# Optimization experiments

Measured on AMD Instinct MI355X. Metric: run time of the kernel, lower is better.

Reference implementation:

```python
import jax, jax.numpy as jnp
import numpy as np

N_NODES = 100000
N_EDGES = 1600000
N_REL = 8
N_HEADS = 4
IN_FEAT = 128
OUT_FEAT = 64
D_HEAD = OUT_FEAT // N_HEADS
LEAKY_SLOPE = 0.2


def setup_inputs() -> dict:
    key = jax.random.key(0)
    ks = jax.random.split(key, 8)
    inputs = jax.random.normal(ks[0], (N_NODES, IN_FEAT), dtype=jnp.float32)
    conv_weights = jax.random.normal(ks[1], (N_REL, N_HEADS, IN_FEAT, D_HEAD), dtype=jnp.float32) * (1.0 / np.sqrt(IN_FEAT))
    attn_l = jax.random.normal(ks[2], (N_REL, N_HEADS, D_HEAD), dtype=jnp.float32) * (1.0 / np.sqrt(D_HEAD))
    attn_r = jax.random.normal(ks[3], (N_REL, N_HEADS, D_HEAD), dtype=jnp.float32) * (1.0 / np.sqrt(D_HEAD))
    h_bias = jax.random.normal(ks[4], (OUT_FEAT,), dtype=jnp.float32)
    src_idx = jax.random.randint(ks[5], (N_EDGES,), 0, N_NODES, dtype=jnp.int64) if jax.config.jax_enable_x64 else jax.random.randint(ks[5], (N_EDGES,), 0, N_NODES, dtype=jnp.int32)
    dst_idx = jax.random.randint(ks[6], (N_EDGES,), 0, N_NODES, dtype=src_idx.dtype)
    rel_idx = jax.random.randint(ks[7], (N_EDGES,), 0, N_REL, dtype=src_idx.dtype)
    return {"inputs": inputs, "conv_weights": conv_weights, "attn_l": attn_l,
            "attn_r": attn_r, "h_bias": h_bias, "src_idx": src_idx,
            "dst_idx": dst_idx, "rel_idx": rel_idx}


def reference(inputs, conv_weights, attn_l, attn_r, h_bias, src_idx, dst_idx, rel_idx):
    N = inputs.shape[0]
    # Per-node per-relation projection: [N, R, H, Dh]
    # (equivalent math to the per-relation grouped matmul over unique nodes)
    proj = jnp.einsum('ni,rhid->nrhd', inputs, conv_weights)
    # Gather per-edge src/dst projected features under the edge's relation: [E, H, Dh]
    feat_src = proj[src_idx, rel_idx]
    feat_dst = proj[dst_idx, rel_idx]
    # Attention logits per edge/head: [E, H]
    el = jnp.sum(feat_src * attn_l[rel_idx], axis=-1)
    er = jnp.sum(feat_dst * attn_r[rel_idx], axis=-1)
    score = jax.nn.leaky_relu(el + er, negative_slope=LEAKY_SLOPE)
    # Edge softmax over incoming edges of each destination node (per head)
    smax = jax.ops.segment_max(score, dst_idx, num_segments=N)        # [N, H]
    e = jnp.exp(score - smax[dst_idx])                                # [E, H]
    denom = jax.ops.segment_sum(e, dst_idx, num_segments=N)          # [N, H]
    alpha = e / denom[dst_idx]                                        # [E, H]
    # Weighted aggregation of src features to dst nodes: [N, H, Dh]
    h = jax.ops.segment_sum(alpha[..., None] * feat_src, dst_idx, num_segments=N)
    h = h.reshape(N, OUT_FEAT) + h_bias
    return h
```

## Files before the change

kernel.cpp:

```cpp
#include <hip/hip_runtime.h>
#include <hip/hip_bf16.h>


#define NN 100000
#define NNP 100096
#define NE 1600000
#define NH 4
#define INF_ 128
#define DH 16
#define NCOL 576
#define LEAKY 0.2f
#define NBUCK 391
#define BSHIFT 8
#define CHUNK 4096
#define CAP 5120
#define GEMM_BLOCKS 782
#define WEXT_BLOCKS 288

typedef __hip_bfloat16 bf16;
typedef __attribute__((ext_vector_type(8))) short bf16x8;
typedef __attribute__((ext_vector_type(4))) short bf16x4;
typedef __attribute__((ext_vector_type(4))) float f32x4;

static __device__ __forceinline__ short f2bs(float x) {
    bf16 b = __float2bfloat16(x);
    return *reinterpret_cast<short*>(&b);
}
static __device__ __forceinline__ float bflo(unsigned u) { return __uint_as_float(u << 16); }
static __device__ __forceinline__ float bfhi(unsigned u) { return __uint_as_float(u & 0xffff0000u); }

__global__ void build_wextT(const float* __restrict__ W, const float* __restrict__ al,
                            const float* __restrict__ ar, short* __restrict__ wxt2,
                            int* __restrict__ gCursor) {
    if (blockIdx.x >= WEXT_BLOCKS) {
        int i = (blockIdx.x - WEXT_BLOCKS) * 256 + threadIdx.x;
        if (i < NBUCK) gCursor[i] = 0;
        return;
    }
    int idx = blockIdx.x * 256 + threadIdx.x;
    int e = idx & 7, lane = (idx >> 3) & 63, ct = (idx >> 9) & 3, ks = (idx >> 11) & 3, cb = idx >> 13;
    int g = lane >> 4, r = lane & 15;
    int c = cb * 64 + ct * 16 + r;
    int k = ks * 32 + g * 8 + e;
    float v;
    if (c < 512) {
        int rr = c >> 6, rem = c & 63, h = rem >> 4, d = rem & 15;
        v = W[((rr * NH + h) * INF_ + k) * DH + d];
    } else {
        int rh = c - 512;
        const float* a = al;
        if (rh >= 32) { rh -= 32; a = ar; }
        int rr = rh >> 2, h = rh & 3;
        const float* wp = &W[((rr * NH + h) * INF_ + k) * DH];
        const float* ap = &a[(rr * NH + h) * DH];
        float s = 0.f;
        #pragma unroll
        for (int d = 0; d < DH; ++d) s += wp[d] * ap[d];
        v = s;
    }
    wxt2[idx] = f2bs(v);
}

__global__ __launch_bounds__(256) void gemm_fused(
    const float* __restrict__ A, const short* __restrict__ WxT2,
    bf16* __restrict__ projR, float* __restrict__ elr,
    const int* __restrict__ src, const int* __restrict__ dst, const int* __restrict__ rel,
    int* __restrict__ gCursor, int* __restrict__ pairbuf) {
    __shared__ short As[16384];
    int t = threadIdx.x;

    if (blockIdx.x >= GEMM_BLOCKS) {
        int* hist = (int*)As;
        int blk = blockIdx.x - GEMM_BLOCKS;
        for (int i = t; i < NBUCK; i += 256) hist[i] = 0;
        __syncthreads();
        int base = blk * CHUNK;
        #pragma unroll
        for (int j = 0; j < CHUNK / 256; ++j) {
            int e = base + j * 256 + t;
            if (e < NE) atomicAdd(&hist[dst[e] >> BSHIFT], 1);
        }
        __syncthreads();
        for (int i = t; i < NBUCK; i += 256) {
            int v = hist[i];
            hist[i] = v ? (i * CAP + atomicAdd(&gCursor[i], v)) : 0;
        }
        __syncthreads();
        #pragma unroll
        for (int j = 0; j < CHUNK / 256; ++j) {
            int e = base + j * 256 + t;
            if (e < NE) {
                int d = dst[e];
                int b = d >> BSHIFT;
                int rec = ((d & 255) << 20) | (src[e] * 8 + rel[e]);
                int pos = atomicAdd(&hist[b], 1);
                pairbuf[pos] = rec;
            }
        }
        return;
    }

    int wv = t >> 6, lane = t & 63;
    int n0 = blockIdx.x * 128;
    int g = lane >> 4, r = lane & 15;

    #pragma unroll
    for (int j = 0; j < 8; ++j) {
        int i = j * 256 + t;
        int row = i >> 4, c8 = i & 15;
        int gr = n0 + row;
        bf16x8 v;
        if (gr < NN) {
            float4 f0 = *(const float4*)&A[gr * INF_ + c8 * 8];
            float4 f1 = *(const float4*)&A[gr * INF_ + c8 * 8 + 4];
            v[0] = f2bs(f0.x); v[1] = f2bs(f0.y); v[2] = f2bs(f0.z); v[3] = f2bs(f0.w);
            v[4] = f2bs(f1.x); v[5] = f2bs(f1.y); v[6] = f2bs(f1.z); v[7] = f2bs(f1.w);
        } else {
            v = (bf16x8)(short)0;
        }
        *(bf16x8*)&As[(row * 16 + (c8 ^ (row & 7))) * 8] = v;
    }
    __syncthreads();

    bf16x8 afr[2][4];
    #pragma unroll
    for (int nt = 0; nt < 2; ++nt) {
        int row = wv * 32 + nt * 16 + r;
        #pragma unroll
        for (int ks = 0; ks < 4; ++ks)
            afr[nt][ks] = *(const bf16x8*)&As[(row * 16 + ((ks * 4 + g) ^ (r & 7))) * 8];
    }
    __syncthreads();
    short* Csh = &As[wv * 4096];
    float* Csf = (float*)Csh;
    int n0w = n0 + wv * 32;

    for (int cb = 0; cb < 9; ++cb) {
        f32x4 acc[2][4] = {};
        #pragma unroll
        for (int ks = 0; ks < 4; ++ks) {
            #pragma unroll
            for (int ct = 0; ct < 4; ++ct) {
                bf16x8 b = *(const bf16x8*)&WxT2[(((cb * 4 + ks) * 4 + ct) * 64 + lane) * 8];
                acc[0][ct] = __builtin_amdgcn_mfma_f32_16x16x32_bf16(b, afr[0][ks], acc[0][ct], 0, 0, 0);
                acc[1][ct] = __builtin_amdgcn_mfma_f32_16x16x32_bf16(b, afr[1][ks], acc[1][ct], 0, 0, 0);
            }
        }
        if (cb < 8) {
            #pragma unroll
            for (int nt = 0; nt < 2; ++nt) {
                int rr = nt * 16 + r;
                #pragma unroll
                for (int ct = 0; ct < 4; ++ct) {
                    bf16x4 p;
                    p[0] = f2bs(acc[nt][ct][0]); p[1] = f2bs(acc[nt][ct][1]);
                    p[2] = f2bs(acc[nt][ct][2]); p[3] = f2bs(acc[nt][ct][3]);
                    *(bf16x4*)&Csh[rr * 64 + (((ct * 4 + g) ^ ((rr & 7) << 1)) << 2)] = p;
                }
            }
            __builtin_amdgcn_wave_barrier();
            size_t base = ((size_t)cb * NN + n0w) * 64;
            #pragma unroll
            for (int q = 0; q < 4; ++q) {
                int rr = (lane >> 3) + q * 8;
                if (n0w + rr < NN) {
                    bf16x8 vv = *(const bf16x8*)&Csh[rr * 64 + (((lane & 7) ^ (rr & 7)) << 3)];
                    *(bf16x8*)&((short*)projR)[base + q * 512 + lane * 8] = vv;
                }
            }
            __builtin_amdgcn_wave_barrier();
        } else {
            #pragma unroll
            for (int nt = 0; nt < 2; ++nt) {
                int rr = nt * 16 + r;
                #pragma unroll
                for (int ct = 0; ct < 4; ++ct)
                    *(f32x4*)&Csf[rr * 64 + (((ct * 4 + g) ^ ((rr & 7) << 1)) << 2)] = acc[nt][ct];
            }
            __builtin_amdgcn_wave_barrier();
            #pragma unroll
            for (int q = 0; q < 8; ++q) {
                int rr = (lane >> 4) + q * 4;
                if (n0w + rr < NN) {
                    f32x4 vv = *(const f32x4*)&Csf[rr * 64 + (((lane & 15) ^ ((rr & 7) << 1)) << 2)];
                    *(f32x4*)&elr[(size_t)n0w * 64 + q * 256 + lane * 4] = vv;
                }
            }
        }
    }
}

__global__ __launch_bounds__(256) void exact_place(
    const int* __restrict__ gCursor, const int* __restrict__ pairbuf,
    int2* __restrict__ offdeg, int2* __restrict__ rec2) {
    __shared__ int hist[256];
    __shared__ int tsum[256];
    int b = blockIdx.x, t = threadIdx.x;
    int start = b * CAP, cnt = gCursor[b];
    hist[t] = 0;
    __syncthreads();
    for (int i = t; i < cnt; i += 256) atomicAdd(&hist[pairbuf[start + i] >> 20], 1);
    __syncthreads();
    int own = hist[t];
    tsum[t] = own;
    __syncthreads();
    for (int st = 1; st < 256; st <<= 1) {
        int y = (t >= st) ? tsum[t - st] : 0;
        __syncthreads();
        tsum[t] += y;
        __syncthreads();
    }
    int excl = start + tsum[t] - own;
    int node = b * 256 + t;
    if (node < NN) offdeg[node] = make_int2(excl, own);
    __syncthreads();
    hist[t] = excl;
    __syncthreads();
    for (int i = t; i < cnt; i += 256) {
        int rec = pairbuf[start + i];
        int pos = atomicAdd(&hist[rec >> 20], 1);
        int sr = rec & 0xFFFFF;
        rec2[pos] = make_int2((sr >> 3) * 64 + (sr & 7) * 4,
                              (sr & 7) * (NN * 64) + (sr >> 3) * 64);
    }
}

__global__ __launch_bounds__(256) void agg(
    const int2* __restrict__ offdeg, const int2* __restrict__ rec2,
    const float* __restrict__ elr, const bf16* __restrict__ projR,
    const float* __restrict__ bias, float* __restrict__ out) {
    __shared__ float s_alpha[4][64][4];
    __shared__ int   s_pidx[4][64];
    __shared__ float s_er[4][32];
    int wv = threadIdx.x >> 6, lane = threadIdx.x & 63;
    int d = blockIdx.x * 4 + wv;
    if (d >= NN) return;
    int2 od = offdeg[d];
    int off = od.x, deg = od.y;
    int end = off + deg;

    if (lane < 32) s_er[wv][lane] = elr[d * 64 + 32 + lane];
    __builtin_amdgcn_wave_barrier();
    asm volatile("s_waitcnt lgkmcnt(0)" ::: "memory");

    if (deg == 0) {
        if (lane < 32) {
            float2 bb = *(const float2*)&bias[lane * 2];
            *(float2*)&out[d * 64 + lane * 2] = bb;
        }
    } else if (deg <= 64) {
        int i = off + lane;
        float e0 = 0.f, e1 = 0.f, e2 = 0.f, e3 = 0.f;
        int pidx = 0;
        if (i < end) {
            int2 rv = rec2[i];
            pidx = rv.y;
            float4 el4 = *(const float4*)&elr[rv.x];
            int erb = rv.x & 63;
            float x;
            x = el4.x + s_er[wv][erb + 0]; x = x > 0.f ? x : LEAKY * x; e0 = __expf(x);
            x = el4.y + s_er[wv][erb + 1]; x = x > 0.f ? x : LEAKY * x; e1 = __expf(x);
            x = el4.z + s_er[wv][erb + 2]; x = x > 0.f ? x : LEAKY * x; e2 = __expf(x);
            x = el4.w + s_er[wv][erb + 3]; x = x > 0.f ? x : LEAKY * x; e3 = __expf(x);
        }
        s_pidx[wv][lane] = pidx;
        *(float4*)&s_alpha[wv][lane][0] = make_float4(e0, e1, e2, e3);
        __builtin_amdgcn_wave_barrier();
        asm volatile("s_waitcnt lgkmcnt(0)" ::: "memory");

        int col2 = (lane & 31) * 2;
        int hl = lane >> 5;
        int h2 = (lane & 31) >> 3;
        float acc0 = 0.f, acc1 = 0.f, dsum = 0.f;
        int j = 0;
        for (; j + 8 <= deg; j += 8) {
            unsigned uu[4];
            #pragma unroll
            for (int p = 0; p < 4; ++p) {
                int myp = s_pidx[wv][j + 2 * p + hl];
                uu[p] = *(const unsigned*)&projR[myp + col2];
            }
            #pragma unroll
            for (int p = 0; p < 4; ++p) {
                float a_self = s_alpha[wv][j + 2 * p + hl][h2];
                float a_oth  = s_alpha[wv][j + 2 * p + 1 - hl][h2];
                unsigned uo = __shfl_xor((int)uu[p], 32);
                acc0 = fmaf(a_self, bflo(uu[p]), acc0);
                acc1 = fmaf(a_self, bfhi(uu[p]), acc1);
                acc0 = fmaf(a_oth, bflo(uo), acc0);
                acc1 = fmaf(a_oth, bfhi(uo), acc1);
                dsum += a_self + a_oth;
            }
        }
        for (; j + 2 <= deg; j += 2) {
            int myp = s_pidx[wv][j + hl];
            unsigned u = *(const unsigned*)&projR[myp + col2];
            float a_self = s_alpha[wv][j + hl][h2];
            float a_oth  = s_alpha[wv][j + 1 - hl][h2];
            unsigned uo = __shfl_xor((int)u, 32);
            acc0 = fmaf(a_self, bflo(u), acc0);
            acc1 = fmaf(a_self, bfhi(u), acc1);
            acc0 = fmaf(a_oth, bflo(uo), acc0);
            acc1 = fmaf(a_oth, bfhi(uo), acc1);
            dsum += a_self + a_oth;
        }
        if (j < deg) {
            int myp = s_pidx[wv][j];
            unsigned u = *(const unsigned*)&projR[myp + col2];
            float a = s_alpha[wv][j][h2];
            acc0 = fmaf(a, bflo(u), acc0);
            acc1 = fmaf(a, bfhi(u), acc1);
            dsum += a;
        }
        if (lane < 32) {
            float inv = 1.0f / dsum;
            float2 bb = *(const float2*)&bias[col2];
            float2 o;
            o.x = acc0 * inv + bb.x;
            o.y = acc1 * inv + bb.y;
            *(float2*)&out[d * 64 + col2] = o;
        }
    } else {
        int c = lane, h = c >> 4;
        float dsum0 = 0.f, dsum1 = 0.f, dsum2 = 0.f, dsum3 = 0.f;
        for (int i = off + lane; i < end; i += 64) {
            int2 rv = rec2[i];
            float4 el4 = *(const float4*)&elr[rv.x];
            int erb = rv.x & 63;
            float x;
            x = el4.x + s_er[wv][erb + 0]; x = x > 0.f ? x : LEAKY * x; dsum0 += __expf(x);
            x = el4.y + s_er[wv][erb + 1]; x = x > 0.f ? x : LEAKY * x; dsum1 += __expf(x);
            x = el4.z + s_er[wv][erb + 2]; x = x > 0.f ? x : LEAKY * x; dsum2 += __expf(x);
            x = el4.w + s_er[wv][erb + 3]; x = x > 0.f ? x : LEAKY * x; dsum3 += __expf(x);
        }
        #pragma unroll
        for (int m = 32; m; m >>= 1) {
            dsum0 += __shfl_xor(dsum0, m, 64);
            dsum1 += __shfl_xor(dsum1, m, 64);
            dsum2 += __shfl_xor(dsum2, m, 64);
            dsum3 += __shfl_xor(dsum3, m, 64);
        }
        float dh = (h == 0) ? dsum0 : (h == 1) ? dsum1 : (h == 2) ? dsum2 : dsum3;
        float rd = 1.0f / dh;
        float acc = 0.f;
        for (int i = off; i < end; ++i) {
            int2 rv = rec2[i];
            float x = elr[rv.x + h] + s_er[wv][(rv.x & 63) + h];
            x = x > 0.f ? x : LEAKY * x;
            acc = fmaf(__expf(x) * rd, __bfloat162float(projR[rv.y + c]), acc);
        }
        out[d * 64 + c] = acc + bias[c];
    }
}

extern "C" void kernel_launch(void* const* d_in, const int* in_sizes, int n_in,
                              void* d_out, int out_size, void* d_ws, size_t ws_size,
                              hipStream_t stream) {
    const float* inputs = (const float*)d_in[0];
    const float* convw  = (const float*)d_in[1];
    const float* attn_l = (const float*)d_in[2];
    const float* attn_r = (const float*)d_in[3];
    const float* h_bias = (const float*)d_in[4];
    const int*   src    = (const int*)d_in[5];
    const int*   dst    = (const int*)d_in[6];
    const int*   rel    = (const int*)d_in[7];
    float* out = (float*)d_out;

    char* ws = (char*)d_ws;
    size_t o = 0;
    bf16* projR = (bf16*)(ws + o);  o += 102400000ull;
    float* elr  = (float*)(ws + o); o += 25600000ull;
    short* wxt2 = (short*)(ws + o); o += 147456;
    int2* offdeg = (int2*)(ws + o); o += 800768;
    int* gCursor = (int*)(ws + o);  o += 2048;
    int* pairbuf = (int*)(ws + o);  o += (size_t)NBUCK * CAP * 4;
    int2* rec2   = (int2*)(ws + o); o += (size_t)NBUCK * CAP * 8;

    hipLaunchKernelGGL(build_wextT, dim3(WEXT_BLOCKS + 2), dim3(256), 0, stream,
                       convw, attn_l, attn_r, wxt2, gCursor);
    hipLaunchKernelGGL(gemm_fused, dim3(GEMM_BLOCKS + NBUCK), dim3(256), 0, stream,
                       inputs, wxt2, projR, elr, src, dst, rel, gCursor, pairbuf);
    hipLaunchKernelGGL(exact_place, dim3(NBUCK), dim3(256), 0, stream, gCursor, pairbuf, offdeg, rec2);
    hipLaunchKernelGGL(agg, dim3(25000), dim3(256), 0, stream, offdeg, rec2, elr, projR, h_bias, out);
}
```

Measured before the change: 142.5 us.

## Store attention logits in bf16 and shrink edge records to one int

The per-node attention logit table (el/er) is now written by the GEMM in bf16 instead of fp32, which halves its footprint and unifies the epilogue path with the projection stores. The per-edge record drops from int2 to a single int, and the aggregation kernel recomputes the projection gather offset from it arithmetically. This cuts write traffic in the GEMM and in edge placement, and read traffic in the aggregation gathers. The cost is lower precision in the softmax logits and a few extra integer ops per edge.

```diff
diff --git a/kernel.cpp b/kernel.cpp
--- a/kernel.cpp
+++ b/kernel.cpp
@@ -28,6 +28,9 @@
 }
 static __device__ __forceinline__ float bflo(unsigned u) { return __uint_as_float(u << 16); }
 static __device__ __forceinline__ float bfhi(unsigned u) { return __uint_as_float(u & 0xffff0000u); }
+static __device__ __forceinline__ float b2f(short us) {
+    return __uint_as_float(((unsigned)(unsigned short)us) << 16);
+}
 
 __global__ void build_wextT(const float* __restrict__ W, const float* __restrict__ al,
                             const float* __restrict__ ar, short* __restrict__ wxt2,
@@ -63,7 +66,7 @@
 
 __global__ __launch_bounds__(256) void gemm_fused(
     const float* __restrict__ A, const short* __restrict__ WxT2,
-    bf16* __restrict__ projR, float* __restrict__ elr,
+    short* __restrict__ projR, short* __restrict__ elrb,
     const int* __restrict__ src, const int* __restrict__ dst, const int* __restrict__ rel,
     int* __restrict__ gCursor, int* __restrict__ pairbuf) {
     __shared__ short As[16384];
@@ -132,7 +135,6 @@
     }
     __syncthreads();
     short* Csh = &As[wv * 4096];
-    float* Csf = (float*)Csh;
     int n0w = n0 + wv * 32;
 
     for (int cb = 0; cb < 9; ++cb) {
@@ -146,53 +148,35 @@
                 acc[1][ct] = __builtin_amdgcn_mfma_f32_16x16x32_bf16(b, afr[1][ks], acc[1][ct], 0, 0, 0);
             }
         }
-        if (cb < 8) {
+        #pragma unroll
+        for (int nt = 0; nt < 2; ++nt) {
+            int rr = nt * 16 + r;
             #pragma unroll
-            for (int nt = 0; nt < 2; ++nt) {
-                int rr = nt * 16 + r;
-                #pragma unroll
-                for (int ct = 0; ct < 4; ++ct) {
-                    bf16x4 p;
-                    p[0] = f2bs(acc[nt][ct][0]); p[1] = f2bs(acc[nt][ct][1]);
-                    p[2] = f2bs(acc[nt][ct][2]); p[3] = f2bs(acc[nt][ct][3]);
-                    *(bf16x4*)&Csh[rr * 64 + (((ct * 4 + g) ^ ((rr & 7) << 1)) << 2)] = p;
-                }
-            }
-            __builtin_amdgcn_wave_barrier();
-            size_t base = ((size_t)cb * NN + n0w) * 64;
-            #pragma unroll
-            for (int q = 0; q < 4; ++q) {
-                int rr = (lane >> 3) + q * 8;
-                if (n0w + rr < NN) {
-                    bf16x8 vv = *(const bf16x8*)&Csh[rr * 64 + (((lane & 7) ^ (rr & 7)) << 3)];
-                    *(bf16x8*)&((short*)projR)[base + q * 512 + lane * 8] = vv;
-                }
-            }
-            __builtin_amdgcn_wave_barrier();
-        } else {
-            #pragma unroll
-            for (int nt = 0; nt < 2; ++nt) {
-                int rr = nt * 16 + r;
-                #pragma unroll
-                for (int ct = 0; ct < 4; ++ct)
-                    *(f32x4*)&Csf[rr * 64 + (((ct * 4 + g) ^ ((rr & 7) << 1)) << 2)] = acc[nt][ct];
-            }
-            __builtin_amdgcn_wave_barrier();
-            #pragma unroll
-            for (int q = 0; q < 8; ++q) {
-                int rr = (lane >> 4) + q * 4;
-                if (n0w + rr < NN) {
-                    f32x4 vv = *(const f32x4*)&Csf[rr * 64 + (((lane & 15) ^ ((rr & 7) << 1)) << 2)];
-                    *(f32x4*)&elr[(size_t)n0w * 64 + q * 256 + lane * 4] = vv;
-                }
-            }
-        }
+            for (int ct = 0; ct < 4; ++ct) {
+                bf16x4 p;
+                p[0] = f2bs(acc[nt][ct][0]); p[1] = f2bs(acc[nt][ct][1]);
+                p[2] = f2bs(acc[nt][ct][2]); p[3] = f2bs(acc[nt][ct][3]);
+                *(bf16x4*)&Csh[rr * 64 + (((ct * 4 + g) ^ ((rr & 7) << 1)) << 2)] = p;
+            }
+        }
+        __builtin_amdgcn_wave_barrier();
+        short* dstbase = (cb < 8) ? &projR[((size_t)cb * NN + n0w) * 64]
+                                  : &elrb[(size_t)n0w * 64];
+        #pragma unroll
+        for (int q = 0; q < 4; ++q) {
+            int rr = (lane >> 3) + q * 8;
+            if (n0w + rr < NN) {
+                bf16x8 vv = *(const bf16x8*)&Csh[rr * 64 + (((lane & 7) ^ (rr & 7)) << 3)];
+                *(bf16x8*)&dstbase[q * 512 + lane * 8] = vv;
+            }
+        }
+        __builtin_amdgcn_wave_barrier();
     }
 }
 
 __global__ __launch_bounds__(256) void exact_place(
     const int* __restrict__ gCursor, const int* __restrict__ pairbuf,
-    int2* __restrict__ offdeg, int2* __restrict__ rec2) {
+    int2* __restrict__ offdeg, int* __restrict__ rec) {
     __shared__ int hist[256];
     __shared__ int tsum[256];
     int b = blockIdx.x, t = threadIdx.x;
@@ -217,17 +201,16 @@
     hist[t] = excl;
     __syncthreads();
     for (int i = t; i < cnt; i += 256) {
-        int rec = pairbuf[start + i];
-        int pos = atomicAdd(&hist[rec >> 20], 1);
-        int sr = rec & 0xFFFFF;
-        rec2[pos] = make_int2((sr >> 3) * 64 + (sr & 7) * 4,
-                              (sr & 7) * (NN * 64) + (sr >> 3) * 64);
+        int rc = pairbuf[start + i];
+        int pos = atomicAdd(&hist[rc >> 20], 1);
+        int sr = rc & 0xFFFFF;
+        rec[pos] = (sr >> 3) * 64 + (sr & 7) * 4;
     }
 }
 
 __global__ __launch_bounds__(256) void agg(
-    const int2* __restrict__ offdeg, const int2* __restrict__ rec2,
-    const float* __restrict__ elr, const bf16* __restrict__ projR,
+    const int2* __restrict__ offdeg, const int* __restrict__ rec,
+    const short* __restrict__ elrb, const bf16* __restrict__ projR,
     const float* __restrict__ bias, float* __restrict__ out) {
     __shared__ float s_alpha[4][64][4];
     __shared__ int   s_pidx[4][64];
@@ -239,7 +222,7 @@
     int off = od.x, deg = od.y;
     int end = off + deg;
 
-    if (lane < 32) s_er[wv][lane] = elr[d * 64 + 32 + lane];
+    if (lane < 32) s_er[wv][lane] = b2f(elrb[d * 64 + 32 + lane]);
     __builtin_amdgcn_wave_barrier();
     asm volatile("s_waitcnt lgkmcnt(0)" ::: "memory");
 
@@ -253,15 +236,15 @@
         float e0 = 0.f, e1 = 0.f, e2 = 0.f, e3 = 0.f;
         int pidx = 0;
         if (i < end) {
-            int2 rv = rec2[i];
-            pidx = rv.y;
-            float4 el4 = *(const float4*)&elr[rv.x];
-            int erb = rv.x & 63;
+            int rv = rec[i];
+            pidx = ((rv & 63) >> 2) * (NN * 64) + (rv >> 6) * 64;
+            bf16x4 el4 = *(const bf16x4*)&elrb[rv];
+            int erb = rv & 63;
             float x;
-            x = el4.x + s_er[wv][erb + 0]; x = x > 0.f ? x : LEAKY * x; e0 = __expf(x);
-            x = el4.y + s_er[wv][erb + 1]; x = x > 0.f ? x : LEAKY * x; e1 = __expf(x);
-            x = el4.z + s_er[wv][erb + 2]; x = x > 0.f ? x : LEAKY * x; e2 = __expf(x);
-            x = el4.w + s_er[wv][erb + 3]; x = x > 0.f ? x : LEAKY * x; e3 = __expf(x);
+            x = b2f(el4[0]) + s_er[wv][erb + 0]; x = x > 0.f ? x : LEAKY * x; e0 = __expf(x);
+            x = b2f(el4[1]) + s_er[wv][erb + 1]; x = x > 0.f ? x : LEAKY * x; e1 = __expf(x);
+            x = b2f(el4[2]) + s_er[wv][erb + 2]; x = x > 0.f ? x : LEAKY * x; e2 = __expf(x);
+            x = b2f(el4[3]) + s_er[wv][erb + 3]; x = x > 0.f ? x : LEAKY * x; e3 = __expf(x);
         }
         s_pidx[wv][lane] = pidx;
         *(float4*)&s_alpha[wv][lane][0] = make_float4(e0, e1, e2, e3);
@@ -324,14 +307,14 @@
         int c = lane, h = c >> 4;
         float dsum0 = 0.f, dsum1 = 0.f, dsum2 = 0.f, dsum3 = 0.f;
         for (int i = off + lane; i < end; i += 64) {
-            int2 rv = rec2[i];
-            float4 el4 = *(const float4*)&elr[rv.x];
-            int erb = rv.x & 63;
+            int rv = rec[i];
+            bf16x4 el4 = *(const bf16x4*)&elrb[rv];
+            int erb = rv & 63;
             float x;
-            x = el4.x + s_er[wv][erb + 0]; x = x > 0.f ? x : LEAKY * x; dsum0 += __expf(x);
-            x = el4.y + s_er[wv][erb + 1]; x = x > 0.f ? x : LEAKY * x; dsum1 += __expf(x);
-            x = el4.z + s_er[wv][erb + 2]; x = x > 0.f ? x : LEAKY * x; dsum2 += __expf(x);
-            x = el4.w + s_er[wv][erb + 3]; x = x > 0.f ? x : LEAKY * x; dsum3 += __expf(x);
+            x = b2f(el4[0]) + s_er[wv][erb + 0]; x = x > 0.f ? x : LEAKY * x; dsum0 += __expf(x);
+            x = b2f(el4[1]) + s_er[wv][erb + 1]; x = x > 0.f ? x : LEAKY * x; dsum1 += __expf(x);
+            x = b2f(el4[2]) + s_er[wv][erb + 2]; x = x > 0.f ? x : LEAKY * x; dsum2 += __expf(x);
+            x = b2f(el4[3]) + s_er[wv][erb + 3]; x = x > 0.f ? x : LEAKY * x; dsum3 += __expf(x);
         }
         #pragma unroll
         for (int m = 32; m; m >>= 1) {
@@ -344,10 +327,11 @@
         float rd = 1.0f / dh;
         float acc = 0.f;
         for (int i = off; i < end; ++i) {
-            int2 rv = rec2[i];
-            float x = elr[rv.x + h] + s_er[wv][(rv.x & 63) + h];
+            int rv = rec[i];
+            int pidx = ((rv & 63) >> 2) * (NN * 64) + (rv >> 6) * 64;
+            float x = b2f(elrb[rv + h]) + s_er[wv][(rv & 63) + h];
             x = x > 0.f ? x : LEAKY * x;
-            acc = fmaf(__expf(x) * rd, __bfloat162float(projR[rv.y + c]), acc);
+            acc = fmaf(__expf(x) * rd, __bfloat162float(projR[pidx + c]), acc);
         }
         out[d * 64 + c] = acc + bias[c];
     }
@@ -368,18 +352,18 @@
 
     char* ws = (char*)d_ws;
     size_t o = 0;
-    bf16* projR = (bf16*)(ws + o);  o += 102400000ull;
-    float* elr  = (float*)(ws + o); o += 25600000ull;
-    short* wxt2 = (short*)(ws + o); o += 147456;
-    int2* offdeg = (int2*)(ws + o); o += 800768;
-    int* gCursor = (int*)(ws + o);  o += 2048;
-    int* pairbuf = (int*)(ws + o);  o += (size_t)NBUCK * CAP * 4;
-    int2* rec2   = (int2*)(ws + o); o += (size_t)NBUCK * CAP * 8;
+    bf16* projR  = (bf16*)(ws + o);  o += 102400000ull;
+    short* elrb  = (short*)(ws + o); o += 12800000ull;
+    short* wxt2  = (short*)(ws + o); o += 147456;
+    int2* offdeg = (int2*)(ws + o);  o += 800768;
+    int* gCursor = (int*)(ws + o);   o += 2048;
+    int* pairbuf = (int*)(ws + o);   o += (size_t)NBUCK * CAP * 4;
+    int* rec     = (int*)(ws + o);   o += (size_t)NBUCK * CAP * 4;
 
     hipLaunchKernelGGL(build_wextT, dim3(WEXT_BLOCKS + 2), dim3(256), 0, stream,
                        convw, attn_l, attn_r, wxt2, gCursor);
     hipLaunchKernelGGL(gemm_fused, dim3(GEMM_BLOCKS + NBUCK), dim3(256), 0, stream,
-                       inputs, wxt2, projR, elr, src, dst, rel, gCursor, pairbuf);
-    hipLaunchKernelGGL(exact_place, dim3(NBUCK), dim3(256), 0, stream, gCursor, pairbuf, offdeg, rec2);
-    hipLaunchKernelGGL(agg, dim3(25000), dim3(256), 0, stream, offdeg, rec2, elr, projR, h_bias, out);
-}
+                       inputs, wxt2, (short*)projR, elrb, src, dst, rel, gCursor, pairbuf);
+    hipLaunchKernelGGL(exact_place, dim3(NBUCK), dim3(256), 0, stream, gCursor, pairbuf, offdeg, rec);
+    hipLaunchKernelGGL(agg, dim3(25000), dim3(256), 0, stream, offdeg, rec, elrb, projR, h_bias, out);
+}
```

Result: faster. 138.8 us (-2.6%).
